# Performance work log

Hardware: AMD Instinct MI355X
Metric: run time of the kernel (lower is better)

## Reference

```python
import jax, jax.numpy as jnp
import numpy as np

NUM_REL = 7
EPS = 1e-5
N, E = 30000, 480000
D_IN, D_H = 21, 512


def _bn(x, g, b):
    # BatchNorm1d over nodes (training-mode batch statistics, biased var like torch)
    mu = x.mean(axis=0)
    var = x.var(axis=0)
    return (x - mu) * jax.lax.rsqrt(var + EPS) * g + b


def _conv(x, src, seg_idx, lin_w, lin_b, self_w, self_b, bn_g, bn_b):
    # GeometricRelationalGraphConv: gather src features, scatter-add per (dst, relation)
    d = x.shape[1]
    msg = x[src]                                                   # (E, d)
    upd = jax.ops.segment_sum(msg, seg_idx, num_segments=N * NUM_REL)
    upd = upd.reshape(N, NUM_REL * d)                              # (N, 7*d)
    out = upd @ lin_w.T + lin_b + x @ self_w.T + self_b            # linear + self-loop
    out = _bn(out, bn_g, bn_b)                                     # conv-internal BN
    return jax.nn.relu(out)


def setup_inputs() -> dict:
    key = jax.random.key(0)
    ks = jax.random.split(key, 16)
    inp = {
        "x": jax.random.normal(ks[0], (N, D_IN), dtype=jnp.float32),
        "src": jax.random.randint(ks[1], (E,), 0, N, dtype=jnp.int32),
        "dst": jax.random.randint(ks[2], (E,), 0, N, dtype=jnp.int32),
        "rel": jax.random.randint(ks[3], (E,), 0, NUM_REL, dtype=jnp.int32),
    }
    dims = [(D_IN, D_H), (D_H, D_H), (D_H, D_H)]
    k = 4
    for i, (din, dout) in enumerate(dims):
        inp[f"lin_w{i}"] = jax.random.normal(ks[k], (dout, NUM_REL * din), dtype=jnp.float32) * 0.05
        inp[f"self_w{i}"] = jax.random.normal(ks[k + 1], (dout, din), dtype=jnp.float32) * 0.05
        k += 2
        inp[f"lin_b{i}"] = jnp.zeros((dout,), jnp.float32)
        inp[f"self_b{i}"] = jnp.zeros((dout,), jnp.float32)
        inp[f"bn1_g{i}"] = jnp.ones((dout,), jnp.float32)
        inp[f"bn1_b{i}"] = jnp.zeros((dout,), jnp.float32)
        inp[f"bn2_g{i}"] = jnp.ones((dout,), jnp.float32)
        inp[f"bn2_b{i}"] = jnp.zeros((dout,), jnp.float32)
    return inp


def reference(x, src, dst, rel,
              lin_w0, lin_b0, self_w0, self_b0, bn1_g0, bn1_b0, bn2_g0, bn2_b0,
              lin_w1, lin_b1, self_w1, self_b1, bn1_g1, bn1_b1, bn2_g1, bn2_b1,
              lin_w2, lin_b2, self_w2, self_b2, bn1_g2, bn1_b2, bn2_g2, bn2_b2):
    seg_idx = dst * NUM_REL + rel                                  # (E,)
    layers = [
        (lin_w0, lin_b0, self_w0, self_b0, bn1_g0, bn1_b0, bn2_g0, bn2_b0),
        (lin_w1, lin_b1, self_w1, self_b1, bn1_g1, bn1_b1, bn2_g1, bn2_b1),
        (lin_w2, lin_b2, self_w2, self_b2, bn1_g2, bn1_b2, bn2_g2, bn2_b2),
    ]
    hiddens = []
    h = x
    for lw, lb, sw, sb, g1, b1, g2, b2 in layers:
        h = _conv(h, src, seg_idx, lw, lb, sw, sb, g1, b1)
        h = _bn(h, g2, b2)                                         # GearNet outer BN
        hiddens.append(h)
    return jnp.concatenate(hiddens, axis=-1)                      # (N, 3*512) concat_hidden
```

## Files before the change

### kernel.cpp

```cpp
#include <hip/hip_runtime.h>

#define NN   30000
#define NE   480000
#define NR   7
#define NSEG (NN*NR)
#define DH   512
#define DIN  21
#define EPSB 1e-5f
#define BK   32
#define KSEG 3584
#define CHMAX 15360

typedef __attribute__((ext_vector_type(8))) short bf16x8;
typedef __attribute__((ext_vector_type(8))) unsigned short u16x8;
typedef __attribute__((ext_vector_type(4))) float f32x4;
typedef unsigned short ushortT;

static inline size_t align256(size_t x){ return (x + 255) & ~(size_t)255; }

__device__ inline float bf2f(ushortT u){
    unsigned int i = ((unsigned int)u) << 16; float f; __builtin_memcpy(&f, &i, 4); return f;
}
__device__ inline ushortT f2bf(float f){
    unsigned int i; __builtin_memcpy(&i, &f, 4);
    unsigned int r = i + 0x7FFFu + ((i >> 16) & 1u);
    return (ushortT)(r >> 16);
}

__device__ inline void load_lds16(const ushortT* g, ushortT* l){
    __builtin_amdgcn_global_load_lds((const __attribute__((address_space(1))) unsigned int*)g,
                                     (__attribute__((address_space(3))) unsigned int*)l,
                                     16, 0, 0);
}


__global__ void hist_k(const int* __restrict__ dst, const int* __restrict__ rel,
                       int* __restrict__ counts){
    int e = blockIdx.x*256 + threadIdx.x;
    if (e < NE) atomicAdd(&counts[dst[e]*NR + rel[e]], 1);
}

__global__ void scan1_k(const int* __restrict__ counts, int* __restrict__ bsum){
    __shared__ int sd[256];
    int t = threadIdx.x;
    int base = blockIdx.x*1024 + t*4;
    int s = 0;
#pragma unroll
    for (int i = 0; i < 4; i++){ int idx = base + i; if (idx < NSEG) s += counts[idx]; }
    sd[t] = s; __syncthreads();
    for (int off = 128; off > 0; off >>= 1){
        if (t < off) sd[t] += sd[t+off];
        __syncthreads();
    }
    if (t == 0) bsum[blockIdx.x] = sd[0];
}

__global__ void scan2_k(int* __restrict__ bsum, int nb, int* __restrict__ seg_start){
    __shared__ int sd[256];
    int t = threadIdx.x;
    int v = (t < nb) ? bsum[t] : 0;
    sd[t] = v; __syncthreads();
    for (int off = 1; off < 256; off <<= 1){
        int x = sd[t];
        if (t >= off) x += sd[t-off];
        __syncthreads();
        sd[t] = x; __syncthreads();
    }
    if (t < nb) bsum[t] = (t == 0) ? 0 : sd[t-1];
    if (t == 0) seg_start[NSEG] = NE;
}

__global__ void scan3_k(const int* __restrict__ counts, const int* __restrict__ bsum,
                        int* __restrict__ seg_start){
    __shared__ int sd[256];
    int t = threadIdx.x;
    int base = blockIdx.x*1024 + t*4;
    int v[4]; int s = 0;
#pragma unroll
    for (int i = 0; i < 4; i++){ int idx = base + i; v[i] = (idx < NSEG) ? counts[idx] : 0; s += v[i]; }
    sd[t] = s; __syncthreads();
    for (int off = 1; off < 256; off <<= 1){
        int x = sd[t];
        if (t >= off) x += sd[t-off];
        __syncthreads();
        sd[t] = x; __syncthreads();
    }
    int excl = sd[t] - s + bsum[blockIdx.x];
#pragma unroll
    for (int i = 0; i < 4; i++){
        int idx = base + i;
        if (idx < NSEG){ seg_start[idx] = excl; excl += v[i]; }
    }
}

__global__ void scatter_k(const int* __restrict__ src, const int* __restrict__ dst,
                          const int* __restrict__ rel, const int* __restrict__ seg_start,
                          int* __restrict__ cursor, int* __restrict__ src_sorted){
    int e = blockIdx.x*256 + threadIdx.x;
    if (e < NE){
        int s = dst[e]*NR + rel[e];
        int pos = seg_start[s] + atomicAdd(&cursor[s], 1);
        src_sorted[pos] = src[e];
    }
}


__global__ void segsum21b_k(const float* __restrict__ x0,
                            const int* __restrict__ seg_start, const int* __restrict__ src_sorted,
                            ushortT* __restrict__ Acat){
    int n = blockIdx.x;
    int t = threadIdx.x;
    ushortT* arow = Acat + (long)n*192;
    if (t < DIN){
        int sb = n*NR;
        int e0 = seg_start[sb];
#pragma unroll
        for (int r = 0; r < NR; r++){
            int e1 = seg_start[sb + r + 1];
            float a = 0.f;
            for (int e = e0; e < e1; e++) a += x0[(long)src_sorted[e]*DIN + t];
            e0 = e1;
            arow[r*DIN + t] = f2bf(a);
        }
        arow[7*DIN + t] = f2bf(x0[(long)n*DIN + t]);
    }
    if (t >= 40) arow[168 + (t - 40)] = 0;
}


__device__ inline void segsum_body(const ushortT* __restrict__ hbf,
                                   const int* __restrict__ seg_start,
                                   const int* __restrict__ src_sorted,
                                   ushortT* __restrict__ Acat,
                                   int wid, int c0, int lane){
    const int n = c0 + wid;
    const int co = lane*8;

    int sb[8];
#pragma unroll
    for (int i = 0; i < 8; i++) sb[i] = seg_start[n*NR + i];

    ushortT* arow = Acat + (long)wid*KSEG + co;
#pragma unroll
    for (int r = 0; r < NR; r++){
        float a[8];
#pragma unroll
        for (int j = 0; j < 8; j++) a[j] = 0.f;
        int e = sb[r], e1 = sb[r+1];
        for (; e + 3 < e1; e += 4){
            u16x8 v0 = *reinterpret_cast<const u16x8*>(hbf + (long)src_sorted[e  ]*DH + co);
            u16x8 v1 = *reinterpret_cast<const u16x8*>(hbf + (long)src_sorted[e+1]*DH + co);
            u16x8 v2 = *reinterpret_cast<const u16x8*>(hbf + (long)src_sorted[e+2]*DH + co);
            u16x8 v3 = *reinterpret_cast<const u16x8*>(hbf + (long)src_sorted[e+3]*DH + co);
#pragma unroll
            for (int j = 0; j < 8; j++)
                a[j] += (bf2f((ushortT)v0[j]) + bf2f((ushortT)v1[j]))
                      + (bf2f((ushortT)v2[j]) + bf2f((ushortT)v3[j]));
        }
        for (; e < e1; e++){
            u16x8 v = *reinterpret_cast<const u16x8*>(hbf + (long)src_sorted[e]*DH + co);
#pragma unroll
            for (int j = 0; j < 8; j++) a[j] += bf2f((ushortT)v[j]);
        }
        u16x8 o;
#pragma unroll
        for (int j = 0; j < 8; j++) o[j] = f2bf(a[j]);
        *reinterpret_cast<u16x8*>(arow + r*DH) = o;
    }
}

__global__ __launch_bounds__(256)
void segsum_wave_k(const ushortT* __restrict__ hbf,
                   const int* __restrict__ seg_start, const int* __restrict__ src_sorted,
                   ushortT* __restrict__ Acat, int c0, int cn){
    int wid = (blockIdx.x*256 + threadIdx.x) >> 6;
    if (wid >= cn) return;
    segsum_body(hbf, seg_start, src_sorted, Acat, wid, c0, threadIdx.x & 63);
}


__global__ void convw_k(const float* __restrict__ lw, const float* __restrict__ sw,
                        int d, int Kp, ushortT* __restrict__ Wc){
    int i = blockIdx.x*256 + threadIdx.x;
    if (i < DH*Kp){
        int n = i / Kp, k = i % Kp;
        float v;
        if (k < 7*d)      v = lw[(long)n*7*d + k];
        else if (k < 8*d) v = sw[(long)n*d + (k - 7*d)];
        else              v = 0.f;
        Wc[i] = f2bf(v);
    }
}


__global__ __launch_bounds__(256)
void gemm_seg_k(int gemmBlocks,
                const ushortT* __restrict__ A, int lda, int ntA,
                const ushortT* __restrict__ hbase, int M,
                const ushortT* __restrict__ W, int ldw,
                const float* __restrict__ b1, const float* __restrict__ b2,
                float* __restrict__ C, int nt, float* __restrict__ sums,
                const ushortT* __restrict__ hbf,
                const int* __restrict__ seg_start, const int* __restrict__ src_sorted,
                ushortT* __restrict__ Acat2, int nc0, int ncn){
    __shared__ ushortT As[3][128*BK];
    __shared__ ushortT Bs[3][ 64*BK];
    const int t = threadIdx.x;

    if ((int)blockIdx.x >= gemmBlocks){
        int wid = ((int)blockIdx.x - gemmBlocks)*4 + (t >> 6);
        if (wid < ncn)
            segsum_body(hbf, seg_start, src_sorted, Acat2, wid, nc0, t & 63);
        return;
    }

    const int nwg = gemmBlocks;
    int q = nwg >> 3, rmd = nwg & 7;
    int xcd = blockIdx.x & 7, slot = blockIdx.x >> 3;
    int l = xcd*q + min(xcd, rmd) + slot;
    const int bm = (l >> 3)*128;
    const int bn = (l & 7)*64;

    const int ar0 = min(bm + (t >> 2), M-1);
    const int ar1 = min(bm + 64 + (t >> 2), M-1);
    const int acu = (t & 3)*8;
    const int brw = bn + (t >> 2);

    f32x4 acc[4][2];
#pragma unroll
    for (int m = 0; m < 4; m++)
#pragma unroll
        for (int n = 0; n < 2; n++) acc[m][n] = (f32x4){0.f,0.f,0.f,0.f};

    const int w = t >> 6;
    const int lane = t & 63;
    const int wm = w >> 1, wn = w & 1;
    const int r = lane & 15, hi = lane >> 4;

    auto stage = [&](int kt, int b){
        const ushortT* p0;
        const ushortT* p1;
        if (kt < ntA){
            p0 = A + (long)ar0*lda + kt*BK + acu;
            p1 = A + (long)ar1*lda + kt*BK + acu;
        } else {
            int k0 = (kt - ntA)*BK;
            p0 = hbase + (long)ar0*DH + k0 + acu;
            p1 = hbase + (long)ar1*DH + k0 + acu;
        }
        load_lds16(p0, &As[b][t*8]);
        load_lds16(p1, &As[b][(t + 256)*8]);
        load_lds16(W + (long)brw*ldw + kt*BK + acu, &Bs[b][t*8]);
    };

    stage(0, 0);
    stage(1, 1);

    for (int kt = 0; kt < nt; ++kt){
        if (kt + 1 < nt) asm volatile("s_waitcnt vmcnt(3)" ::: "memory");
        else             asm volatile("s_waitcnt vmcnt(0)" ::: "memory");
        __builtin_amdgcn_s_barrier();
        __builtin_amdgcn_sched_barrier(0);
        if (kt + 2 < nt) stage(kt + 2, (kt + 2) % 3);
        const int buf = kt % 3;
        bf16x8 af[4], bfr[2];
#pragma unroll
        for (int m = 0; m < 4; m++)
            af[m] = *reinterpret_cast<const bf16x8*>(&As[buf][(wm*64 + m*16 + r)*BK + hi*8]);
#pragma unroll
        for (int n = 0; n < 2; n++)
            bfr[n] = *reinterpret_cast<const bf16x8*>(&Bs[buf][(wn*32 + n*16 + r)*BK + hi*8]);
#pragma unroll
        for (int m = 0; m < 4; m++)
#pragma unroll
            for (int n = 0; n < 2; n++)
                acc[m][n] = __builtin_amdgcn_mfma_f32_16x16x32_bf16(af[m], bfr[n], acc[m][n], 0, 0, 0);
    }

#pragma unroll
    for (int n = 0; n < 2; n++){
        int col = bn + wn*32 + n*16 + r;
        float bb = b1[col] + b2[col];
        float s = 0.f, s2 = 0.f;
#pragma unroll
        for (int m = 0; m < 4; m++){
            int row = bm + wm*64 + m*16 + hi*4;
#pragma unroll
            for (int q2 = 0; q2 < 4; q2++){
                if (row + q2 < M){
                    float v = acc[m][n][q2] + bb;
                    C[(long)(row + q2)*DH + col] = v;
                    s += v; s2 = fmaf(v, v, s2);
                }
            }
        }
        s  += __shfl_xor(s, 16);  s  += __shfl_xor(s, 32);
        s2 += __shfl_xor(s2, 16); s2 += __shfl_xor(s2, 32);
        if (hi == 0){
            atomicAdd(&sums[col], s);
            atomicAdd(&sums[DH + col], s2);
        }
    }
}


__global__ void finalize_k(const float* __restrict__ sums, const float* __restrict__ g,
                           const float* __restrict__ b, float* __restrict__ ac){
    int c = blockIdx.x*256 + threadIdx.x;
    if (c < DH){
        float mu  = sums[c] * (1.f/NN);
        float var = sums[DH + c] * (1.f/NN) - mu*mu;
        var = fmaxf(var, 0.f);
        float a = g[c] * rsqrtf(var + EPSB);
        ac[c]      = a;
        ac[DH + c] = fmaf(-mu, a, b[c]);
    }
}

__global__ void bnrelu_k(float* __restrict__ buf, int M, const float* __restrict__ ac,
                         float* __restrict__ sums2){
    int col = blockIdx.x*256 + threadIdx.x;
    int r0 = blockIdx.y*128;
    int r1 = min(r0 + 128, M);
    float a = ac[col], c = ac[DH + col];
    float s = 0.f, s2 = 0.f;
    for (int r = r0; r < r1; r++){
        long idx = (long)r*DH + col;
        float y = fmaxf(fmaf(a, buf[idx], c), 0.f);
        buf[idx] = y;
        s += y; s2 = fmaf(y, y, s2);
    }
    atomicAdd(&sums2[col], s);
    atomicAdd(&sums2[DH + col], s2);
}

__global__ void bn2write_k(const float* __restrict__ buf, const float* __restrict__ ac,
                           float* __restrict__ out, ushortT* __restrict__ hbf, int layer){
    long i = (long)blockIdx.x*256 + threadIdx.x;
    if (i < (long)NN*DH){
        int r = (int)(i >> 9);
        int c = (int)(i & 511);
        float h = fmaf(ac[c], buf[i], ac[DH + c]);
        out[(long)r*(3*DH) + layer*DH + c] = h;
        hbf[i] = f2bf(h);
    }
}


extern "C" void kernel_launch(void* const* d_in, const int* in_sizes, int n_in,
                              void* d_out, int out_size, void* d_ws, size_t ws_size,
                              hipStream_t stream){
    const float* x0  = (const float*)d_in[0];
    const int*   src = (const int*)d_in[1];
    const int*   dst = (const int*)d_in[2];
    const int*   rel = (const int*)d_in[3];
    const float* lin_w[3]  = {(const float*)d_in[4],  (const float*)d_in[12], (const float*)d_in[20]};
    const float* self_w[3] = {(const float*)d_in[5],  (const float*)d_in[13], (const float*)d_in[21]};
    const float* lin_b[3]  = {(const float*)d_in[6],  (const float*)d_in[14], (const float*)d_in[22]};
    const float* self_b[3] = {(const float*)d_in[7],  (const float*)d_in[15], (const float*)d_in[23]};
    const float* bn1_g[3]  = {(const float*)d_in[8],  (const float*)d_in[16], (const float*)d_in[24]};
    const float* bn1_b[3]  = {(const float*)d_in[9],  (const float*)d_in[17], (const float*)d_in[25]};
    const float* bn2_g[3]  = {(const float*)d_in[10], (const float*)d_in[18], (const float*)d_in[26]};
    const float* bn2_b[3]  = {(const float*)d_in[11], (const float*)d_in[19], (const float*)d_in[27]};

    char* ws = (char*)d_ws;
    size_t off = 0;
    auto alloc = [&](size_t bytes)->char*{ char* p = ws + off; off = align256(off + bytes); return p; };

    int*     counts     = (int*)alloc((size_t)NSEG*4);
    int*     cursor     = (int*)alloc((size_t)NSEG*4);
    int*     seg_start  = (int*)alloc((size_t)(NSEG+1)*4);
    int*     bsum       = (int*)alloc(1024*4);
    int*     src_sorted = (int*)alloc((size_t)NE*4);
    float*   stats      = (float*)alloc((size_t)8*DH*4);
    float*   sums1 = stats;            float* sums2 = stats + 2*DH;
    float*   ac1   = stats + 4*DH;     float* ac2   = stats + 6*DH;
    float*   outbuf = (float*)alloc((size_t)NN*DH*4);
    ushortT* hbf    = (ushortT*)alloc((size_t)NN*DH*2);
    ushortT* Wcat   = (ushortT*)alloc((size_t)DH*4096*2);
    ushortT* Acat0  = (ushortT*)alloc((size_t)NN*192*2);

    size_t remain = (ws_size > off) ? (ws_size - off) : 0;
    long max_nodes = (long)(remain / (2*(size_t)KSEG*2));
    int chunk = (int)((max_nodes > CHMAX) ? CHMAX : max_nodes);
    chunk &= ~127;
    if (chunk < 128) chunk = 128;
    ushortT* AcatA = (ushortT*)(ws + off);
    ushortT* AcatB = AcatA + (size_t)chunk*KSEG;
    ushortT* AcatBuf[2] = {AcatA, AcatB};

    hipMemsetAsync(counts, 0, (size_t)NSEG*4, stream);
    hipMemsetAsync(cursor, 0, (size_t)NSEG*4, stream);
    hist_k<<<(NE+255)/256, 256, 0, stream>>>(dst, rel, counts);
    int nb = (NSEG + 1023)/1024;
    scan1_k<<<nb, 256, 0, stream>>>(counts, bsum);
    scan2_k<<<1, 256, 0, stream>>>(bsum, nb, seg_start);
    scan3_k<<<nb, 256, 0, stream>>>(counts, bsum, seg_start);
    scatter_k<<<(NE+255)/256, 256, 0, stream>>>(src, dst, rel, seg_start, cursor, src_sorted);

    const int MB = (NN + 127)/128;
    const int nch = (NN + chunk - 1)/chunk;

    for (int layer = 0; layer < 3; layer++){
        int d  = (layer == 0) ? DIN : DH;
        int Kp = (layer == 0) ? 192 : 8*DH;
        convw_k<<<(DH*Kp + 255)/256, 256, 0, stream>>>(lin_w[layer], self_w[layer], d, Kp, Wcat);
        hipMemsetAsync(stats, 0, (size_t)4*DH*4, stream);

        if (layer == 0){
            segsum21b_k<<<NN, 64, 0, stream>>>(x0, seg_start, src_sorted, Acat0);
            gemm_seg_k<<<MB*8, 256, 0, stream>>>(
                MB*8, Acat0, 192, 6, Acat0, NN, Wcat, 192,
                lin_b[layer], self_b[layer], outbuf, 6, sums1,
                hbf, seg_start, src_sorted, (ushortT*)nullptr, 0, 0);
        } else {
            int cn0 = (NN < chunk) ? NN : chunk;
            segsum_wave_k<<<(cn0 + 3)/4, 256, 0, stream>>>(
                hbf, seg_start, src_sorted, AcatBuf[0], 0, cn0);
            for (int i = 0; i < nch; i++){
                int cc0 = i*chunk;
                int ccn = (NN - cc0 < chunk) ? (NN - cc0) : chunk;
                int gemmBlocks = ((ccn + 127)/128)*8;
                int segBlocks = 0, nc0 = 0, ncn = 0;
                ushortT* An = nullptr;
                if (i + 1 < nch){
                    nc0 = (i + 1)*chunk;
                    ncn = (NN - nc0 < chunk) ? (NN - nc0) : chunk;
                    segBlocks = (ncn + 3)/4;
                    An = AcatBuf[(i + 1) & 1];
                }
                gemm_seg_k<<<gemmBlocks + segBlocks, 256, 0, stream>>>(
                    gemmBlocks, AcatBuf[i & 1], KSEG, 112, hbf + (long)cc0*DH, ccn,
                    Wcat, 4096, lin_b[layer], self_b[layer],
                    outbuf + (long)cc0*DH, 128, sums1,
                    hbf, seg_start, src_sorted, An, nc0, ncn);
            }
        }

        finalize_k<<<2, 256, 0, stream>>>(sums1, bn1_g[layer], bn1_b[layer], ac1);
        bnrelu_k<<<dim3(2, (NN+127)/128), 256, 0, stream>>>(outbuf, NN, ac1, sums2);
        finalize_k<<<2, 256, 0, stream>>>(sums2, bn2_g[layer], bn2_b[layer], ac2);
        bn2write_k<<<((long)NN*DH + 255)/256, 256, 0, stream>>>(outbuf, ac2, (float*)d_out, hbf, layer);
    }
}
```

Baseline: 1.040 ms.

## Enlarge GEMM tile to 128x128 and store pre-BN activations in bf16

The GEMM block tile grows from 128x64 to 128x128. Each wave now computes a 64x64 sub-tile with a 4x4 MFMA accumulator grid, which halves the number of GEMM blocks and the redundant reloads of the A operand. The intermediate pre-BatchNorm buffer changes from fp32 to bf16, and the BN statistics are taken from the rounded values, to halve traffic in the GEMM epilogue, bnrelu and bn2write. The costs are higher register and LDS use, which may lower occupancy, and an extra bf16 rounding of intermediates that lowers accuracy.

```diff
diff --git a/kernel.cpp b/kernel.cpp
--- a/kernel.cpp
+++ b/kernel.cpp
@@ -199,12 +199,12 @@
                 const ushortT* __restrict__ hbase, int M,
                 const ushortT* __restrict__ W, int ldw,
                 const float* __restrict__ b1, const float* __restrict__ b2,
-                float* __restrict__ C, int nt, float* __restrict__ sums,
+                ushortT* __restrict__ C, int nt, float* __restrict__ sums,
                 const ushortT* __restrict__ hbf,
                 const int* __restrict__ seg_start, const int* __restrict__ src_sorted,
                 ushortT* __restrict__ Acat2, int nc0, int ncn){
     __shared__ ushortT As[3][128*BK];
-    __shared__ ushortT Bs[3][ 64*BK];
+    __shared__ ushortT Bs[3][128*BK];
     const int t = threadIdx.x;
 
     if ((int)blockIdx.x >= gemmBlocks){
@@ -218,22 +218,25 @@
     int q = nwg >> 3, rmd = nwg & 7;
     int xcd = blockIdx.x & 7, slot = blockIdx.x >> 3;
     int l = xcd*q + min(xcd, rmd) + slot;
-    const int bm = (l >> 3)*128;
-    const int bn = (l & 7)*64;
-
-    const int ar0 = min(bm + (t >> 2), M-1);
-    const int ar1 = min(bm + 64 + (t >> 2), M-1);
-    const int acu = (t & 3)*8;
-    const int brw = bn + (t >> 2);
-
-    f32x4 acc[4][2];
+    const int bm = (l >> 2)*128;
+    const int bn = (l & 3)*128;
+
+    const int w    = t >> 6;
+    const int lane = t & 63;
+
+    int f0 = w*128 + lane, f1 = f0 + 64;
+    const int ar0 = min(bm + (f0 >> 2), M-1), ac0 = (f0 & 3)*8;
+    const int ar1 = min(bm + (f1 >> 2), M-1), ac1 = (f1 & 3)*8;
+    const int br0 = bn + (f0 >> 2), br1 = bn + (f1 >> 2);
+    const int d0 = (w*128 +  0)*8;
+    const int d1 = (w*128 + 64)*8;
+
+    f32x4 acc[4][4];
 #pragma unroll
     for (int m = 0; m < 4; m++)
 #pragma unroll
-        for (int n = 0; n < 2; n++) acc[m][n] = (f32x4){0.f,0.f,0.f,0.f};
-
-    const int w = t >> 6;
-    const int lane = t & 63;
+        for (int n = 0; n < 4; n++) acc[m][n] = (f32x4){0.f,0.f,0.f,0.f};
+
     const int wm = w >> 1, wn = w & 1;
     const int r = lane & 15, hi = lane >> 4;
 
@@ -241,45 +244,46 @@
         const ushortT* p0;
         const ushortT* p1;
         if (kt < ntA){
-            p0 = A + (long)ar0*lda + kt*BK + acu;
-            p1 = A + (long)ar1*lda + kt*BK + acu;
+            p0 = A + (long)ar0*lda + kt*BK + ac0;
+            p1 = A + (long)ar1*lda + kt*BK + ac1;
         } else {
             int k0 = (kt - ntA)*BK;
-            p0 = hbase + (long)ar0*DH + k0 + acu;
-            p1 = hbase + (long)ar1*DH + k0 + acu;
-        }
-        load_lds16(p0, &As[b][t*8]);
-        load_lds16(p1, &As[b][(t + 256)*8]);
-        load_lds16(W + (long)brw*ldw + kt*BK + acu, &Bs[b][t*8]);
+            p0 = hbase + (long)ar0*DH + k0 + ac0;
+            p1 = hbase + (long)ar1*DH + k0 + ac1;
+        }
+        load_lds16(p0, &As[b][d0]);
+        load_lds16(p1, &As[b][d1]);
+        load_lds16(W + (long)br0*ldw + kt*BK + ac0, &Bs[b][d0]);
+        load_lds16(W + (long)br1*ldw + kt*BK + ac1, &Bs[b][d1]);
     };
 
     stage(0, 0);
-    stage(1, 1);
+    if (nt > 1) stage(1, 1);
 
     for (int kt = 0; kt < nt; ++kt){
-        if (kt + 1 < nt) asm volatile("s_waitcnt vmcnt(3)" ::: "memory");
+        if (kt + 1 < nt) asm volatile("s_waitcnt vmcnt(4)" ::: "memory");
         else             asm volatile("s_waitcnt vmcnt(0)" ::: "memory");
         __builtin_amdgcn_s_barrier();
         __builtin_amdgcn_sched_barrier(0);
         if (kt + 2 < nt) stage(kt + 2, (kt + 2) % 3);
         const int buf = kt % 3;
-        bf16x8 af[4], bfr[2];
+        bf16x8 af[4], bfr[4];
 #pragma unroll
         for (int m = 0; m < 4; m++)
             af[m] = *reinterpret_cast<const bf16x8*>(&As[buf][(wm*64 + m*16 + r)*BK + hi*8]);
 #pragma unroll
-        for (int n = 0; n < 2; n++)
-            bfr[n] = *reinterpret_cast<const bf16x8*>(&Bs[buf][(wn*32 + n*16 + r)*BK + hi*8]);
+        for (int n = 0; n < 4; n++)
+            bfr[n] = *reinterpret_cast<const bf16x8*>(&Bs[buf][(wn*64 + n*16 + r)*BK + hi*8]);
 #pragma unroll
         for (int m = 0; m < 4; m++)
 #pragma unroll
-            for (int n = 0; n < 2; n++)
+            for (int n = 0; n < 4; n++)
                 acc[m][n] = __builtin_amdgcn_mfma_f32_16x16x32_bf16(af[m], bfr[n], acc[m][n], 0, 0, 0);
     }
 
 #pragma unroll
-    for (int n = 0; n < 2; n++){
-        int col = bn + wn*32 + n*16 + r;
+    for (int n = 0; n < 4; n++){
+        int col = bn + wn*64 + n*16 + r;
         float bb = b1[col] + b2[col];
         float s = 0.f, s2 = 0.f;
 #pragma unroll
@@ -288,9 +292,10 @@
 #pragma unroll
             for (int q2 = 0; q2 < 4; q2++){
                 if (row + q2 < M){
-                    float v = acc[m][n][q2] + bb;
-                    C[(long)(row + q2)*DH + col] = v;
-                    s += v; s2 = fmaf(v, v, s2);
+                    ushortT u = f2bf(acc[m][n][q2] + bb);
+                    C[(long)(row + q2)*DH + col] = u;
+                    float vr = bf2f(u);
+                    s += vr; s2 = fmaf(vr, vr, s2);
                 }
             }
         }
@@ -317,7 +322,7 @@
     }
 }
 
-__global__ void bnrelu_k(float* __restrict__ buf, int M, const float* __restrict__ ac,
+__global__ void bnrelu_k(ushortT* __restrict__ buf, int M, const float* __restrict__ ac,
                          float* __restrict__ sums2){
     int col = blockIdx.x*256 + threadIdx.x;
     int r0 = blockIdx.y*128;
@@ -326,21 +331,23 @@
     float s = 0.f, s2 = 0.f;
     for (int r = r0; r < r1; r++){
         long idx = (long)r*DH + col;
-        float y = fmaxf(fmaf(a, buf[idx], c), 0.f);
-        buf[idx] = y;
-        s += y; s2 = fmaf(y, y, s2);
+        float y = fmaxf(fmaf(a, bf2f(buf[idx]), c), 0.f);
+        ushortT u = f2bf(y);
+        buf[idx] = u;
+        float yr = bf2f(u);
+        s += yr; s2 = fmaf(yr, yr, s2);
     }
     atomicAdd(&sums2[col], s);
     atomicAdd(&sums2[DH + col], s2);
 }
 
-__global__ void bn2write_k(const float* __restrict__ buf, const float* __restrict__ ac,
+__global__ void bn2write_k(const ushortT* __restrict__ buf, const float* __restrict__ ac,
                            float* __restrict__ out, ushortT* __restrict__ hbf, int layer){
     long i = (long)blockIdx.x*256 + threadIdx.x;
     if (i < (long)NN*DH){
         int r = (int)(i >> 9);
         int c = (int)(i & 511);
-        float h = fmaf(ac[c], buf[i], ac[DH + c]);
+        float h = fmaf(ac[c], bf2f(buf[i]), ac[DH + c]);
         out[(long)r*(3*DH) + layer*DH + c] = h;
         hbf[i] = f2bf(h);
     }
@@ -375,7 +382,7 @@
     float*   stats      = (float*)alloc((size_t)8*DH*4);
     float*   sums1 = stats;            float* sums2 = stats + 2*DH;
     float*   ac1   = stats + 4*DH;     float* ac2   = stats + 6*DH;
-    float*   outbuf = (float*)alloc((size_t)NN*DH*4);
+    ushortT* outbuf = (ushortT*)alloc((size_t)NN*DH*2);
     ushortT* hbf    = (ushortT*)alloc((size_t)NN*DH*2);
     ushortT* Wcat   = (ushortT*)alloc((size_t)DH*4096*2);
     ushortT* Acat0  = (ushortT*)alloc((size_t)NN*192*2);
@@ -409,8 +416,8 @@
 
         if (layer == 0){
             segsum21b_k<<<NN, 64, 0, stream>>>(x0, seg_start, src_sorted, Acat0);
-            gemm_seg_k<<<MB*8, 256, 0, stream>>>(
-                MB*8, Acat0, 192, 6, Acat0, NN, Wcat, 192,
+            gemm_seg_k<<<MB*4, 256, 0, stream>>>(
+                MB*4, Acat0, 192, 6, Acat0, NN, Wcat, 192,
                 lin_b[layer], self_b[layer], outbuf, 6, sums1,
                 hbf, seg_start, src_sorted, (ushortT*)nullptr, 0, 0);
         } else {
@@ -420,7 +427,7 @@
             for (int i = 0; i < nch; i++){
                 int cc0 = i*chunk;
                 int ccn = (NN - cc0 < chunk) ? (NN - cc0) : chunk;
-                int gemmBlocks = ((ccn + 127)/128)*8;
+                int gemmBlocks = ((ccn + 127)/128)*4;
                 int segBlocks = 0, nc0 = 0, ncn = 0;
                 ushortT* An = nullptr;
                 if (i + 1 < nch){
```

New measurement: 968.2 us. 6.9% less time.
